# Kernel optimization log

Hardware: AMD Instinct MI355X
Metric: run time of the kernel (lower is better)

The kernel has to match this reference:

```python
import jax, jax.numpy as jnp
import numpy as np

B, D, O = 256, 4096, 16384


def setup_inputs() -> dict:
    key = jax.random.key(0)
    k1, k2, k3, k4 = jax.random.split(key, 4)
    x1 = jax.random.normal(k1, (B, D), dtype=jnp.float32)
    x2 = jax.random.normal(k2, (B, D), dtype=jnp.float32)
    # random hash buckets in [0, O) and random +/-1 signs (homogeneous: shared by both inputs)
    h1 = jax.random.randint(k3, (D,), 0, O, dtype=jnp.int32)
    s1 = jnp.where(jax.random.uniform(k4, (D,)) < 0.5, -1.0, 1.0).astype(jnp.float32)
    return {"x1": x1, "x2": x2, "h1": h1, "s1": s1, "output_size": O}


def reference(x1, x2, h1, s1, output_size):
    # psi(): count-sketch via sign-multiply + scatter-add along feature axis
    batch = x1.shape[0]
    y1 = jnp.zeros((batch, output_size), x1.dtype).at[:, h1].add(s1 * x1)  # [B, O]
    y2 = jnp.zeros((batch, output_size), x2.dtype).at[:, h1].add(s1 * x2)  # [B, O]
    # conv(): circular convolution of the two sketches via FFT pointwise product
    out = jnp.fft.ifft(jnp.fft.fft(y1, axis=-1) * jnp.fft.fft(y2, axis=-1), axis=-1)
    return out.real.astype(x1.dtype)
```

## Files before the change

### kernel.cpp

```cpp
#include <hip/hip_runtime.h>


typedef float v2 __attribute__((ext_vector_type(2)));

#define N1      8192
#define BLOCK   1024
#define DIM     4096
#define PI_F    3.14159265358979323846f
#define RS2     0.70710678118654752f
#define SLOT(e) ((e) ^ (((e) >> 4) & 15))
#define REV13(x) ((int)(__brev((unsigned)(x)) >> 19))
#define WAVE_FENCE() __asm__ volatile("s_waitcnt lgkmcnt(0)" ::: "memory")

static __device__ __forceinline__ v2 cmul(v2 a, v2 b) {
    return a.xx * b + (v2){-a.y, a.y} * b.yx;
}
static __device__ __forceinline__ v2 csqr(v2 a) { return cmul(a, a); }
static __device__ __forceinline__ v2 expi(float phi) {
    float s, c; __sincosf(phi, &s, &c); return (v2){c, s};
}

static __device__ __forceinline__ void fft8_dif(v2* r, float phi) {
    v2 W2 = expi(phi), W1 = csqr(W2), W0 = csqr(W1);
    v2 W[3] = {W0, W1, W2};
    #pragma unroll
    for (int p = 2; p >= 0; --p) {
        #pragma unroll
        for (int h = 0; h < 4; ++h) {
            const int jp = h & ((1 << p) - 1);
            const int j  = ((h >> p) << (p + 1)) | jp;
            const int ci = jp << (2 - p);
            v2 Wp = W[p], T;
            if (ci == 0)      T = Wp;
            else if (ci == 2) T = (v2){Wp.y, -Wp.x};
            else if (ci == 1) T = cmul(Wp, (v2){RS2, -RS2});
            else              T = cmul(Wp, (v2){-RS2, -RS2});
            v2 a = r[j], bb = r[j + (1 << p)];
            r[j] = a + bb;
            r[j + (1 << p)] = cmul(a - bb, T);
        }
    }
}

static __device__ __forceinline__ void fft8_dit(v2* r, float phi) {
    v2 W2 = expi(phi), W1 = csqr(W2), W0 = csqr(W1);
    v2 W[3] = {W0, W1, W2};
    #pragma unroll
    for (int p = 0; p <= 2; ++p) {
        #pragma unroll
        for (int h = 0; h < 4; ++h) {
            const int jp = h & ((1 << p) - 1);
            const int j  = ((h >> p) << (p + 1)) | jp;
            const int ci = jp << (2 - p);
            v2 Wp = W[p], T;
            if (ci == 0)      T = Wp;
            else if (ci == 2) T = (v2){-Wp.y, Wp.x};
            else if (ci == 1) T = cmul(Wp, (v2){RS2, RS2});
            else              T = cmul(Wp, (v2){-RS2, RS2});
            v2 a = r[j], bb = cmul(r[j + (1 << p)], T);
            r[j]            = a + bb;
            r[j + (1 << p)] = a - bb;
        }
    }
}

static __device__ __forceinline__ void fft8_dit0(v2* r) {
    #pragma unroll
    for (int p = 0; p <= 2; ++p) {
        #pragma unroll
        for (int h = 0; h < 4; ++h) {
            const int jp = h & ((1 << p) - 1);
            const int j  = ((h >> p) << (p + 1)) | jp;
            const int ci = jp << (2 - p);
            v2 x = r[j + (1 << p)], bb;
            if (ci == 0)      bb = x;
            else if (ci == 2) bb = (v2){-x.y, x.x};
            else if (ci == 1) bb = cmul(x, (v2){RS2, RS2});
            else              bb = cmul(x, (v2){-RS2, RS2});
            v2 a = r[j];
            r[j] = a + bb; r[j + (1 << p)] = a - bb;
        }
    }
}

static __device__ __forceinline__ void fft4_difW(v2* r, v2 W1) {
    v2 W0 = csqr(W1);
    v2 a, bb;
    a = r[0]; bb = r[2]; r[0] = a + bb; r[2] = cmul(a - bb, W1);
    a = r[1]; bb = r[3]; r[1] = a + bb;
    { v2 d = a - bb; r[3] = cmul(d, (v2){W1.y, -W1.x}); }
    a = r[0]; bb = r[1]; r[0] = a + bb; r[1] = cmul(a - bb, W0);
    a = r[2]; bb = r[3]; r[2] = a + bb; r[3] = cmul(a - bb, W0);
}
static __device__ __forceinline__ void fft4_dif0(v2* r) {
    v2 a, bb;
    a = r[0]; bb = r[2]; r[0] = a + bb; r[2] = a - bb;
    a = r[1]; bb = r[3]; r[1] = a + bb;
    { v2 d = a - bb; r[3] = (v2){d.y, -d.x}; }
    a = r[0]; bb = r[1]; r[0] = a + bb; r[1] = a - bb;
    a = r[2]; bb = r[3]; r[2] = a + bb; r[3] = a - bb;
}

static __device__ __forceinline__ void pair_slot(v2* zz, int j) {
    const int k  = REV13(j);
    const int kp = (N1 - k) & (N1 - 1);
    const int j2 = REV13(kp);
    v2 A = zz[SLOT(j)], B = zz[SLOT(j2)];
    v2 C = zz[N1 + SLOT(j)], D = zz[N1 + SLOT(j2)];
    v2 E  = (v2){0.5f * (A.x + B.x),  0.5f * (A.y - B.y)};
    v2 O  = (v2){0.5f * (A.y + B.y), -0.5f * (A.x - B.x)};
    v2 F  = (v2){0.5f * (C.x + D.x),  0.5f * (C.y - D.y)};
    v2 Ov = (v2){0.5f * (C.y + D.y), -0.5f * (C.x - D.x)};
    v2 Tm = expi(-PI_F * (float)k * (1.f / 8192.f));
    v2 u = cmul(Tm, O), v = cmul(Tm, Ov);
    v2 G = cmul(E + u, F + v);
    v2 H = cmul(E - u, F - v);
    v2 S  = (v2){0.5f * (G.x + H.x), 0.5f * (G.y + H.y)};
    v2 gh = G - H;
    v2 t2 = cmul((v2){Tm.x, -Tm.y}, gh);
    v2 Dv = (v2){-0.5f * t2.y, 0.5f * t2.x};
    zz[SLOT(j)]  = S + Dv;
    zz[SLOT(j2)] = (v2){S.x - Dv.x, -(S.y - Dv.y)};
}

__launch_bounds__(BLOCK, 4)
__global__ void cbp_fft_kernel(const float* __restrict__ x1,
                               const float* __restrict__ x2,
                               const int* __restrict__ h1,
                               const float* __restrict__ s1,
                               float* __restrict__ out) {
    __shared__ v2 zz[2 * N1];
    const int tid = threadIdx.x;
    const int l   = tid & 63;
    const int b   = blockIdx.x;
    float* zf = (float*)zz;

    const float* x1r = x1 + (size_t)b * DIM;
    const float* x2r = x2 + (size_t)b * DIM;
    float sv[DIM / BLOCK], a1[DIM / BLOCK], a2[DIM / BLOCK];
    int   hv[DIM / BLOCK];
    #pragma unroll
    for (int i = 0; i < DIM / BLOCK; ++i) {
        int d = tid + (i << 10);
        sv[i] = s1[d];
        hv[i] = h1[d];
        a1[i] = x1r[d];
        a2[i] = x2r[d];
    }

    #pragma unroll
    for (int j = 0; j < 16; ++j) zz[tid + (j << 10)] = (v2){0.f, 0.f};
    __syncthreads();

    #pragma unroll
    for (int i = 0; i < DIM / BLOCK; ++i) {
        int  h  = hv[i];
        int  fi = (SLOT(h >> 1) << 1) | (h & 1);
        atomicAdd(&zf[fi], sv[i] * a1[i]);
        atomicAdd(&zf[2 * N1 + fi], sv[i] * a2[i]);
    }
    __syncthreads();

    const int half = tid >> 9;
    const int tt   = tid & 511;
    const int hw   = tt >> 6;
    v2* Ah = zz + half * N1;

    #pragma unroll 1
    for (int q = 0; q < 2; ++q) {
        int k  = tt + (q << 9);
        int bs = k ^ ((k >> 4) & 15);
        v2 r[8];
        #pragma unroll
        for (int j = 0; j < 8; ++j) r[j] = Ah[bs + (j << 10)];
        fft8_dif(r, (float)k * (-PI_F / 4096.f));
        #pragma unroll
        for (int j = 0; j < 8; ++j) Ah[bs + (j << 10)] = r[j];
    }
    __syncthreads();

    #pragma unroll 1
    for (int q = 0; q < 2; ++q) {
        int kk = (tt & 63) + (q << 6);
        int bE = ((hw << 10) + kk) ^ (kk >> 4);
        int bO = bE ^ 8;
        v2 r[8];
        #pragma unroll
        for (int j = 0; j < 8; ++j) r[j] = Ah[((j & 1) ? bO : bE) + (j << 7)];
        fft8_dif(r, (float)kk * (-PI_F / 512.f));
        #pragma unroll
        for (int j = 0; j < 8; ++j) Ah[((j & 1) ? bO : bE) + (j << 7)] = r[j];
    }
    WAVE_FENCE();

    #pragma unroll 1
    for (int q = 0; q < 2; ++q) {
        int g  = (hw << 3) + ((l >> 4) << 1) + q;
        int kf = l & 15;
        int a0 = (g << 7) + (kf ^ (q << 3));
        v2 r[8];
        #pragma unroll
        for (int j = 0; j < 8; ++j) r[j] = Ah[(a0 ^ j) + (j << 4)];
        fft8_dif(r, (float)kf * (-PI_F / 64.f));
        #pragma unroll
        for (int j = 0; j < 8; ++j) Ah[(a0 ^ j) + (j << 4)] = r[j];
    }
    WAVE_FENCE();

    {
        const int span  = (hw << 6) + (l & 15) + ((l >> 4) << 4);
        const int sbase = (span << 4) + (span & 15);
        #pragma unroll 1
        for (int k4 = 0; k4 < 4; ++k4) {
            float c = (k4 & 1) ? ((k4 & 2) ? 0.38268343f : 0.92387953f)
                               : ((k4 & 2) ? 0.70710678f : 1.f);
            float s = (k4 & 1) ? ((k4 & 2) ? -0.92387953f : -0.38268343f)
                               : ((k4 & 2) ? -0.70710678f : 0.f);
            int sb = sbase ^ k4;
            v2 r[4];
            #pragma unroll
            for (int j = 0; j < 4; ++j) r[j] = Ah[sb ^ (j << 2)];
            fft4_difW(r, (v2){c, s});
            #pragma unroll
            for (int j = 0; j < 4; ++j) Ah[sb ^ (j << 2)] = r[j];
        }
        WAVE_FENCE();
        #pragma unroll 1
        for (int q = 0; q < 4; ++q) {
            int sb = sbase ^ (q << 2);
            v2 r[4];
            #pragma unroll
            for (int j = 0; j < 4; ++j) r[j] = Ah[sb ^ j];
            fft4_dif0(r);
            #pragma unroll
            for (int j = 0; j < 4; ++j) Ah[sb ^ j] = r[j];
        }
    }
    __syncthreads();

    #pragma unroll 1
    for (int i = 0; i < 4; ++i) pair_slot(zz, (tid + (i << 10)) << 1);
    if (tid == 0) pair_slot(zz, 1);
    __syncthreads();

    {
        int B1 = (tid << 3) ^ ((tid >> 1) & 15);
        v2 r[8];
        #pragma unroll
        for (int i = 0; i < 8; ++i) r[i] = zz[B1 ^ i];
        fft8_dit0(r);
        #pragma unroll
        for (int i = 0; i < 8; ++i) zz[B1 ^ i] = r[i];
    }
    WAVE_FENCE();
    {
        int g = tid >> 3, k = tid & 7;
        int base = (g << 6) + k;
        v2 r[8];
        #pragma unroll
        for (int j = 0; j < 8; ++j) r[j] = zz[SLOT(base + (j << 3))];
        fft8_dit(r, (float)k * (PI_F / 32.f));
        #pragma unroll
        for (int j = 0; j < 8; ++j) zz[SLOT(base + (j << 3))] = r[j];
    }
    WAVE_FENCE();
    {
        int k = tid & 63;
        int base0 = ((tid >> 6) << 9) + (k & ~15);
        int Kh = k >> 4, K15 = k & 15;
        int B0  = base0 + (K15 ^ Kh);
        int Bm1 = base0 + (K15 ^ (Kh + 4));
        int Bm2 = base0 + (K15 ^ (Kh + 8));
        int Bm3 = base0 + (K15 ^ (Kh + 12));
        v2 r[8];
        r[0] = zz[B0];        r[1] = zz[Bm1 + 64];
        r[2] = zz[Bm2 + 128]; r[3] = zz[Bm3 + 192];
        r[4] = zz[B0 + 256];  r[5] = zz[Bm1 + 320];
        r[6] = zz[Bm2 + 384]; r[7] = zz[Bm3 + 448];
        fft8_dit(r, (float)k * (PI_F / 256.f));
        zz[B0]        = r[0]; zz[Bm1 + 64]  = r[1];
        zz[Bm2 + 128] = r[2]; zz[Bm3 + 192] = r[3];
        zz[B0 + 256]  = r[4]; zz[Bm1 + 320] = r[5];
        zz[Bm2 + 384] = r[6]; zz[Bm3 + 448] = r[7];
    }
    __syncthreads();
    {
        int g = tid >> 9, k = tid & 511;
        int bp = ((g << 12) + k) ^ ((k >> 4) & 15);
        v2 r[8];
        #pragma unroll
        for (int j = 0; j < 8; ++j) r[j] = zz[bp + (j << 9)];
        fft8_dit(r, (float)k * (PI_F / 2048.f));
        #pragma unroll
        for (int j = 0; j < 8; ++j) zz[bp + (j << 9)] = r[j];
    }
    __syncthreads();

    float* outr = out + (size_t)b * (2 * N1);
    const float inv_n1 = 1.0f / (float)N1;
    const int b5 = (tid << 2) ^ ((tid >> 2) & 15);
    #pragma unroll 1
    for (int i = 0; i < 2; ++i) {
        v2 lo[2], hi[2];
        #pragma unroll
        for (int s2 = 0; s2 < 2; ++s2) {
            int d5 = (i << 1) + s2;
            int n  = (tid << 2) + d5;
            v2 a  = zz[b5 ^ d5];
            v2 bb = zz[(b5 ^ d5) + 4096];
            v2 T  = expi(PI_F * (float)n * (1.f / 4096.f));
            v2 tb = cmul(T, bb);
            lo[s2] = a + tb;
            hi[s2] = a - tb;
        }
        float4 vlo = make_float4(lo[0].x * inv_n1, lo[0].y * inv_n1,
                                 lo[1].x * inv_n1, lo[1].y * inv_n1);
        float4 vhi = make_float4(hi[0].x * inv_n1, hi[0].y * inv_n1,
                                 hi[1].x * inv_n1, hi[1].y * inv_n1);
        *(float4*)(outr + (tid << 3) + (i << 2)) = vlo;
        *(float4*)(outr + N1 + (tid << 3) + (i << 2)) = vhi;
    }
}

extern "C" void kernel_launch(void* const* d_in, const int* in_sizes, int n_in,
                              void* d_out, int out_size, void* d_ws, size_t ws_size,
                              hipStream_t stream) {
    const float* x1 = (const float*)d_in[0];
    const float* x2 = (const float*)d_in[1];
    const int*   h1 = (const int*)d_in[2];
    const float* s1 = (const float*)d_in[3];
    float* out = (float*)d_out;
    const int B = in_sizes[0] / DIM;
    cbp_fft_kernel<<<B, BLOCK, 0, stream>>>(x1, x2, h1, s1, out);
}
```

Baseline: 94.21 us.

## Fuse radix-4 stages in registers, vectorize LDS zeroing, use twiddle recurrence in output

Several independent micro-optimizations. The two radix-4 passes of the forward FFT now run on 16 values held in registers, which removes an intermediate LDS store, reload and wave fence. The LDS clearing uses float4 stores instead of float2, and the pair_slot loop is unrolled by two. The output stage is fully unrolled and replaces per-element sincos with one sincos plus complex-multiply recurrence steps, which adds register pressure and slight rounding drift in the twiddles.

```diff
diff --git a/kernel.cpp b/kernel.cpp
--- a/kernel.cpp
+++ b/kernel.cpp
@@ -83,22 +83,22 @@
     }
 }
 
-static __device__ __forceinline__ void fft4_difW(v2* r, v2 W1) {
+static __device__ __forceinline__ void fft4_difW4(v2& r0, v2& r1, v2& r2, v2& r3, v2 W1) {
     v2 W0 = csqr(W1);
     v2 a, bb;
-    a = r[0]; bb = r[2]; r[0] = a + bb; r[2] = cmul(a - bb, W1);
-    a = r[1]; bb = r[3]; r[1] = a + bb;
-    { v2 d = a - bb; r[3] = cmul(d, (v2){W1.y, -W1.x}); }
-    a = r[0]; bb = r[1]; r[0] = a + bb; r[1] = cmul(a - bb, W0);
-    a = r[2]; bb = r[3]; r[2] = a + bb; r[3] = cmul(a - bb, W0);
-}
-static __device__ __forceinline__ void fft4_dif0(v2* r) {
+    a = r0; bb = r2; r0 = a + bb; r2 = cmul(a - bb, W1);
+    a = r1; bb = r3; r1 = a + bb;
+    { v2 d = a - bb; r3 = cmul(d, (v2){W1.y, -W1.x}); }
+    a = r0; bb = r1; r0 = a + bb; r1 = cmul(a - bb, W0);
+    a = r2; bb = r3; r2 = a + bb; r3 = cmul(a - bb, W0);
+}
+static __device__ __forceinline__ void fft4_dif04(v2& r0, v2& r1, v2& r2, v2& r3) {
     v2 a, bb;
-    a = r[0]; bb = r[2]; r[0] = a + bb; r[2] = a - bb;
-    a = r[1]; bb = r[3]; r[1] = a + bb;
-    { v2 d = a - bb; r[3] = (v2){d.y, -d.x}; }
-    a = r[0]; bb = r[1]; r[0] = a + bb; r[1] = a - bb;
-    a = r[2]; bb = r[3]; r[2] = a + bb; r[3] = a - bb;
+    a = r0; bb = r2; r0 = a + bb; r2 = a - bb;
+    a = r1; bb = r3; r1 = a + bb;
+    { v2 d = a - bb; r3 = (v2){d.y, -d.x}; }
+    a = r0; bb = r1; r0 = a + bb; r1 = a - bb;
+    a = r2; bb = r3; r2 = a + bb; r3 = a - bb;
 }
 
 static __device__ __forceinline__ void pair_slot(v2* zz, int j) {
@@ -148,8 +148,11 @@
         a2[i] = x2r[d];
     }
 
-    #pragma unroll
-    for (int j = 0; j < 16; ++j) zz[tid + (j << 10)] = (v2){0.f, 0.f};
+    {
+        float4* z4 = (float4*)zz;
+        #pragma unroll
+        for (int j = 0; j < 8; ++j) z4[tid + (j << 10)] = make_float4(0.f, 0.f, 0.f, 0.f);
+    }
     __syncthreads();
 
     #pragma unroll
@@ -210,35 +213,26 @@
     {
         const int span  = (hw << 6) + (l & 15) + ((l >> 4) << 4);
         const int sbase = (span << 4) + (span & 15);
-        #pragma unroll 1
+        v2 R[16];
+        #pragma unroll
+        for (int m = 0; m < 16; ++m) R[m] = Ah[sbase ^ m];
+        #pragma unroll
         for (int k4 = 0; k4 < 4; ++k4) {
             float c = (k4 & 1) ? ((k4 & 2) ? 0.38268343f : 0.92387953f)
                                : ((k4 & 2) ? 0.70710678f : 1.f);
             float s = (k4 & 1) ? ((k4 & 2) ? -0.92387953f : -0.38268343f)
                                : ((k4 & 2) ? -0.70710678f : 0.f);
-            int sb = sbase ^ k4;
-            v2 r[4];
-            #pragma unroll
-            for (int j = 0; j < 4; ++j) r[j] = Ah[sb ^ (j << 2)];
-            fft4_difW(r, (v2){c, s});
-            #pragma unroll
-            for (int j = 0; j < 4; ++j) Ah[sb ^ (j << 2)] = r[j];
-        }
-        WAVE_FENCE();
-        #pragma unroll 1
-        for (int q = 0; q < 4; ++q) {
-            int sb = sbase ^ (q << 2);
-            v2 r[4];
-            #pragma unroll
-            for (int j = 0; j < 4; ++j) r[j] = Ah[sb ^ j];
-            fft4_dif0(r);
-            #pragma unroll
-            for (int j = 0; j < 4; ++j) Ah[sb ^ j] = r[j];
-        }
-    }
-    __syncthreads();
-
-    #pragma unroll 1
+            fft4_difW4(R[k4], R[k4 + 4], R[k4 + 8], R[k4 + 12], (v2){c, s});
+        }
+        #pragma unroll
+        for (int q = 0; q < 4; ++q)
+            fft4_dif04(R[4 * q], R[4 * q + 1], R[4 * q + 2], R[4 * q + 3]);
+        #pragma unroll
+        for (int m = 0; m < 16; ++m) Ah[sbase ^ m] = R[m];
+    }
+    __syncthreads();
+
+    #pragma unroll 2
     for (int i = 0; i < 4; ++i) pair_slot(zz, (tid + (i << 10)) << 1);
     if (tid == 0) pair_slot(zz, 1);
     __syncthreads();
@@ -296,29 +290,34 @@
     }
     __syncthreads();
 
-    float* outr = out + (size_t)b * (2 * N1);
-    const float inv_n1 = 1.0f / (float)N1;
-    const int b5 = (tid << 2) ^ ((tid >> 2) & 15);
-    #pragma unroll 1
-    for (int i = 0; i < 2; ++i) {
-        v2 lo[2], hi[2];
-        #pragma unroll
-        for (int s2 = 0; s2 < 2; ++s2) {
-            int d5 = (i << 1) + s2;
-            int n  = (tid << 2) + d5;
+    {
+        float* outr = out + (size_t)b * (2 * N1);
+        const float inv_n1 = 1.0f / (float)N1;
+        const int b5 = (tid << 2) ^ ((tid >> 2) & 15);
+        v2 Tn = expi(PI_F * (float)(tid << 2) * (1.f / 4096.f));
+        const v2 STEP = (v2){0.99999970586288f, 7.6699031874270e-4f};
+        v2 lo[4], hi[4];
+        #pragma unroll
+        for (int d5 = 0; d5 < 4; ++d5) {
             v2 a  = zz[b5 ^ d5];
             v2 bb = zz[(b5 ^ d5) + 4096];
-            v2 T  = expi(PI_F * (float)n * (1.f / 4096.f));
-            v2 tb = cmul(T, bb);
-            lo[s2] = a + tb;
-            hi[s2] = a - tb;
-        }
-        float4 vlo = make_float4(lo[0].x * inv_n1, lo[0].y * inv_n1,
-                                 lo[1].x * inv_n1, lo[1].y * inv_n1);
-        float4 vhi = make_float4(hi[0].x * inv_n1, hi[0].y * inv_n1,
-                                 hi[1].x * inv_n1, hi[1].y * inv_n1);
-        *(float4*)(outr + (tid << 3) + (i << 2)) = vlo;
-        *(float4*)(outr + N1 + (tid << 3) + (i << 2)) = vhi;
+            v2 tb = cmul(Tn, bb);
+            lo[d5] = a + tb;
+            hi[d5] = a - tb;
+            if (d5 < 3) Tn = cmul(Tn, STEP);
+        }
+        float4 vlo0 = make_float4(lo[0].x * inv_n1, lo[0].y * inv_n1,
+                                  lo[1].x * inv_n1, lo[1].y * inv_n1);
+        float4 vlo1 = make_float4(lo[2].x * inv_n1, lo[2].y * inv_n1,
+                                  lo[3].x * inv_n1, lo[3].y * inv_n1);
+        float4 vhi0 = make_float4(hi[0].x * inv_n1, hi[0].y * inv_n1,
+                                  hi[1].x * inv_n1, hi[1].y * inv_n1);
+        float4 vhi1 = make_float4(hi[2].x * inv_n1, hi[2].y * inv_n1,
+                                  hi[3].x * inv_n1, hi[3].y * inv_n1);
+        *(float4*)(outr + (tid << 3))          = vlo0;
+        *(float4*)(outr + (tid << 3) + 4)      = vlo1;
+        *(float4*)(outr + N1 + (tid << 3))     = vhi0;
+        *(float4*)(outr + N1 + (tid << 3) + 4) = vhi1;
     }
 }
 
```

After: 92.10 us. -2.2%, faster.
